# Kernel tuning notes

Hardware: AMD Instinct MI355X
Metric: run time of the kernel (lower is better)

## Reference

```python
import jax, jax.numpy as jnp
import numpy as np

N_NODES = 100000


def _graph_conv_right(feat, src, dst, W, b, n_nodes):
    # DGL GraphConv(norm='right'): since in_feats > out_feats, apply weight first,
    # then sum-aggregate messages over edges, divide by in-degree (clamped >= 1),
    # add bias, then relu activation.
    h = feat @ W                                   # [N, out]
    msg = jnp.take(h, src, axis=0)                 # [E, out] gather from source nodes
    agg = jax.ops.segment_sum(msg, dst, num_segments=n_nodes)  # [N, out]
    deg = jax.ops.segment_sum(jnp.ones_like(dst, dtype=feat.dtype), dst,
                              num_segments=n_nodes)
    deg = jnp.clip(deg, 1.0, None)                 # allow_zero_in_degree
    out = agg / deg[:, None] + b
    return jax.nn.relu(out)


def setup_inputs() -> dict:
    key = jax.random.key(0)
    ks = jax.random.split(key, 6)
    n_edges = 3200000
    in_dim, hidden_dim, out_dim = 128, 32, 12
    features = jax.random.normal(ks[0], (N_NODES, in_dim), dtype=jnp.float32)
    src = jax.random.randint(ks[1], (n_edges,), 0, N_NODES, dtype=jnp.int64 if jax.config.jax_enable_x64 else jnp.int32)
    dst = jax.random.randint(ks[2], (n_edges,), 0, N_NODES, dtype=jnp.int64 if jax.config.jax_enable_x64 else jnp.int32)
    W1 = jax.random.normal(ks[3], (in_dim, hidden_dim), dtype=jnp.float32) * (1.0 / np.sqrt(in_dim))
    b1 = jnp.zeros((hidden_dim,), dtype=jnp.float32)
    W2 = jax.random.normal(ks[4], (hidden_dim, out_dim), dtype=jnp.float32) * (1.0 / np.sqrt(hidden_dim))
    b2 = jnp.zeros((out_dim,), dtype=jnp.float32)
    return {"features": features, "src": src, "dst": dst,
            "W1": W1, "b1": b1, "W2": W2, "b2": b2}


def reference(features, src, dst, W1, b1, W2, b2):
    x = _graph_conv_right(features, src, dst, W1, b1, N_NODES)
    x = jax.nn.relu(x)  # extra F.relu after layer1 (idempotent, kept for fidelity)
    x = _graph_conv_right(x, src, dst, W2, b2, N_NODES)
    return x
```

## Files before the change

kernel.cpp:

```cpp
#include <hip/hip_runtime.h>
#include <hip/hip_fp16.h>

#define N_IN   128
#define HID    32
#define ODIM   12
#define RNODES 128
#define NBMAX  800
#define BCAP   4608
#define CHUNK  8192

__global__ __launch_bounds__(256) void gemm1_kernel(const float* __restrict__ feat,
                                                    const float* __restrict__ W1,
                                                    __half* __restrict__ h1, int nNodes) {
    __shared__ float sF[64 * 132];
    __shared__ float sW[N_IN * HID];
    const int tid = threadIdx.x;
    const int nb  = blockIdx.x * 64;

    {
        const float4* Wv  = (const float4*)W1;
        float4*       sWv = (float4*)sW;
        #pragma unroll
        for (int i = 0; i < 4; ++i) sWv[tid + 256 * i] = Wv[tid + 256 * i];
    }
    #pragma unroll
    for (int i = 0; i < 8; ++i) {
        int f   = tid + 256 * i;
        int row = f >> 5;
        int c4  = f & 31;
        int n   = nb + row;
        float4 v = make_float4(0.f, 0.f, 0.f, 0.f);
        if (n < nNodes) v = *(const float4*)(feat + (size_t)n * N_IN + c4 * 4);
        *(float4*)(sF + row * 132 + c4 * 4) = v;
    }
    __syncthreads();

    const int og = tid & 7;
    const int ng = tid >> 3;
    const int o0 = og * 4;
    const float* f0 = sF + ng * 132;
    const float* f1 = sF + (ng + 32) * 132;

    float acc0[4] = {0.f, 0.f, 0.f, 0.f};
    float acc1[4] = {0.f, 0.f, 0.f, 0.f};
    #pragma unroll 8
    for (int k = 0; k < N_IN; k += 4) {
        float4 a0 = *(const float4*)(f0 + k);
        float4 a1 = *(const float4*)(f1 + k);
        const float a0v[4] = {a0.x, a0.y, a0.z, a0.w};
        const float a1v[4] = {a1.x, a1.y, a1.z, a1.w};
        #pragma unroll
        for (int j = 0; j < 4; ++j) {
            float4 w = *(const float4*)(sW + (k + j) * HID + o0);
            acc0[0] += a0v[j] * w.x; acc0[1] += a0v[j] * w.y;
            acc0[2] += a0v[j] * w.z; acc0[3] += a0v[j] * w.w;
            acc1[0] += a1v[j] * w.x; acc1[1] += a1v[j] * w.y;
            acc1[2] += a1v[j] * w.z; acc1[3] += a1v[j] * w.w;
        }
    }
    int n0 = nb + ng, n1 = nb + ng + 32;
    if (n0 < nNodes) {
        union { __half2 h[2]; float2 f; } u;
        u.h[0] = __floats2half2_rn(acc0[0], acc0[1]);
        u.h[1] = __floats2half2_rn(acc0[2], acc0[3]);
        *(float2*)(h1 + (size_t)n0 * HID + o0) = u.f;
    }
    if (n1 < nNodes) {
        union { __half2 h[2]; float2 f; } u;
        u.h[0] = __floats2half2_rn(acc1[0], acc1[1]);
        u.h[1] = __floats2half2_rn(acc1[2], acc1[3]);
        *(float2*)(h1 + (size_t)n1 * HID + o0) = u.f;
    }
}

__global__ __launch_bounds__(256) void bplace_kernel(const int* __restrict__ src,
                                                     const int* __restrict__ dst,
                                                     int* __restrict__ bcur,
                                                     int* __restrict__ pairs, int nEdges) {
    __shared__ int lh[NBMAX];
    const int tid  = threadIdx.x;
    const int base = blockIdx.x * CHUNK;

    for (int b = tid; b < NBMAX; b += 256) lh[b] = 0;
    __syncthreads();

    #pragma unroll
    for (int j = 0; j < CHUNK / 1024; ++j) {
        int e = base + j * 1024 + tid * 4;
        if (e < nEdges) {
            int4 d = *(const int4*)(dst + e);
            atomicAdd(&lh[d.x >> 7], 1);
            atomicAdd(&lh[d.y >> 7], 1);
            atomicAdd(&lh[d.z >> 7], 1);
            atomicAdd(&lh[d.w >> 7], 1);
        }
    }
    __syncthreads();

    for (int b = tid; b < NBMAX; b += 256) {
        int c = lh[b];
        lh[b] = (c > 0) ? atomicAdd(&bcur[b], c) : 0;
    }
    __syncthreads();

    #pragma unroll
    for (int j = 0; j < CHUNK / 1024; ++j) {
        int e = base + j * 1024 + tid * 4;
        if (e < nEdges) {
            int4 d = *(const int4*)(dst + e);
            int4 s = *(const int4*)(src + e);
            int b0 = d.x >> 7, b1 = d.y >> 7, b2 = d.z >> 7, b3 = d.w >> 7;
            int p0 = atomicAdd(&lh[b0], 1);
            int p1 = atomicAdd(&lh[b1], 1);
            int p2 = atomicAdd(&lh[b2], 1);
            int p3 = atomicAdd(&lh[b3], 1);
            if (p0 < BCAP) pairs[(size_t)b0 * BCAP + p0] = ((d.x & 127) << 17) | s.x;
            if (p1 < BCAP) pairs[(size_t)b1 * BCAP + p1] = ((d.y & 127) << 17) | s.y;
            if (p2 < BCAP) pairs[(size_t)b2 * BCAP + p2] = ((d.z & 127) << 17) | s.z;
            if (p3 < BCAP) pairs[(size_t)b3 * BCAP + p3] = ((d.w & 127) << 17) | s.w;
        }
    }
}

__global__ __launch_bounds__(256) void bsort_kernel(const int* __restrict__ bcur,
                                                    int* __restrict__ pairs,
                                                    int* __restrict__ rowstart,
                                                    int* __restrict__ countg, int nNodes) {
    __shared__ int lp[BCAP];
    __shared__ int hist[RNODES];
    __shared__ int scn[RNODES];
    __shared__ int cur[RNODES];
    const int tid = threadIdx.x;
    const int bkt = blockIdx.x;
    const int cnt = min(bcur[bkt], BCAP);
    const size_t pb = (size_t)bkt * BCAP;

    if (tid < RNODES) hist[tid] = 0;
    __syncthreads();

    for (int i = tid; i < cnt; i += 256) {
        int v = pairs[pb + i];
        lp[i] = v;
        atomicAdd(&hist[v >> 17], 1);
    }
    __syncthreads();

    int v0 = (tid < RNODES) ? hist[tid] : 0;
    if (tid < RNODES) scn[tid] = v0;
    __syncthreads();
    int inc = v0;
    for (int off = 1; off < RNODES; off <<= 1) {
        int t = (tid < RNODES && tid >= off) ? scn[tid - off] : 0;
        __syncthreads();
        if (tid < RNODES) { inc += t; scn[tid] = inc; }
        __syncthreads();
    }
    if (tid < RNODES) {
        int excl = inc - v0;
        cur[tid] = excl;
        int n = bkt * RNODES + tid;
        if (n < nNodes) {
            rowstart[n] = (int)(pb + excl);
            countg[n]   = v0;
        }
    }
    __syncthreads();

    for (int i = tid; i < cnt; i += 256) {
        int v = lp[i];
        int pos = atomicAdd(&cur[v >> 17], 1);
        pairs[pb + pos] = v & 0x1FFFF;
    }
}

__global__ __launch_bounds__(256) void agg1_kernel(const __half* __restrict__ h1,
                                                   const int* __restrict__ rowstart,
                                                   const int* __restrict__ countg,
                                                   const int* __restrict__ eidx,
                                                   const float* __restrict__ b1,
                                                   const float* __restrict__ W2,
                                                   __half* __restrict__ h2,
                                                   float* __restrict__ rdeg, int nNodes) {
    __shared__ float sW2[HID * ODIM];
    const int tid = threadIdx.x;
    if (tid < 96) ((float4*)sW2)[tid] = ((const float4*)W2)[tid];
    __syncthreads();

    const int n = blockIdx.x * 16 + (tid >> 4);
    const int c = tid & 15;
    if (n >= nNodes) return;

    const int cnt = countg[n];
    const int beg = rowstart[n];
    const int end = beg + cnt;
    const __half2* h1v = (const __half2*)h1;

    float2 s0 = {0.f, 0.f}, s1 = {0.f, 0.f}, s2 = {0.f, 0.f}, s3 = {0.f, 0.f};
    int i = beg;
    for (; i + 4 <= end; i += 4) {
        int e0 = eidx[i], e1 = eidx[i + 1], e2 = eidx[i + 2], e3 = eidx[i + 3];
        float2 f0 = __half22float2(h1v[(size_t)e0 * 16 + c]);
        float2 f1 = __half22float2(h1v[(size_t)e1 * 16 + c]);
        float2 f2 = __half22float2(h1v[(size_t)e2 * 16 + c]);
        float2 f3 = __half22float2(h1v[(size_t)e3 * 16 + c]);
        s0.x += f0.x; s0.y += f0.y;
        s1.x += f1.x; s1.y += f1.y;
        s2.x += f2.x; s2.y += f2.y;
        s3.x += f3.x; s3.y += f3.y;
    }
    for (; i < end; ++i) {
        float2 f = __half22float2(h1v[(size_t)eidx[i] * 16 + c]);
        s0.x += f.x; s0.y += f.y;
    }
    float sumx = (s0.x + s1.x) + (s2.x + s3.x);
    float sumy = (s0.y + s1.y) + (s2.y + s3.y);

    float rd = 1.f / (float)(cnt < 1 ? 1 : cnt);
    float x0 = sumx * rd + b1[2 * c];
    float x1 = sumy * rd + b1[2 * c + 1];
    x0 = x0 > 0.f ? x0 : 0.f;
    x1 = x1 > 0.f ? x1 : 0.f;

    const int col = (c < ODIM) ? c : 0;
    float acc = 0.f;
    #pragma unroll
    for (int k = 0; k < 16; ++k) {
        float xk0 = __shfl(x0, k, 16);
        float xk1 = __shfl(x1, k, 16);
        acc += xk0 * sW2[(2 * k) * ODIM + col] + xk1 * sW2[(2 * k + 1) * ODIM + col];
    }
    if (c < ODIM) h2[(size_t)n * ODIM + c] = __float2half(acc);
    if (c == 0)   rdeg[n] = rd;
}

__global__ __launch_bounds__(256) void agg2_kernel(const __half* __restrict__ h2,
                                                   const int* __restrict__ rowstart,
                                                   const int* __restrict__ countg,
                                                   const int* __restrict__ eidx,
                                                   const float* __restrict__ rdeg,
                                                   const float* __restrict__ b2,
                                                   float* __restrict__ out, int nNodes) {
    const int tid = threadIdx.x;
    const int n = blockIdx.x * 32 + (tid >> 3);
    const int c = tid & 7;
    if (n >= nNodes) return;

    const int cnt = countg[n];
    const int beg = rowstart[n];
    const int end = beg + cnt;
    const int cc = (c < 6) ? c : 0;
    const __half2* h2v = (const __half2*)h2;

    float2 s0 = {0.f, 0.f}, s1 = {0.f, 0.f}, s2 = {0.f, 0.f}, s3 = {0.f, 0.f};
    int i = beg;
    for (; i + 4 <= end; i += 4) {
        int e0 = eidx[i], e1 = eidx[i + 1], e2 = eidx[i + 2], e3 = eidx[i + 3];
        float2 f0 = __half22float2(h2v[(size_t)e0 * 6 + cc]);
        float2 f1 = __half22float2(h2v[(size_t)e1 * 6 + cc]);
        float2 f2 = __half22float2(h2v[(size_t)e2 * 6 + cc]);
        float2 f3 = __half22float2(h2v[(size_t)e3 * 6 + cc]);
        s0.x += f0.x; s0.y += f0.y;
        s1.x += f1.x; s1.y += f1.y;
        s2.x += f2.x; s2.y += f2.y;
        s3.x += f3.x; s3.y += f3.y;
    }
    for (; i < end; ++i) {
        float2 f = __half22float2(h2v[(size_t)eidx[i] * 6 + cc]);
        s0.x += f.x; s0.y += f.y;
    }
    float sumx = (s0.x + s1.x) + (s2.x + s3.x);
    float sumy = (s0.y + s1.y) + (s2.y + s3.y);

    float rd = rdeg[n];
    float v0 = sumx * rd + b2[2 * cc];
    float v1 = sumy * rd + b2[2 * cc + 1];
    v0 = v0 > 0.f ? v0 : 0.f;
    v1 = v1 > 0.f ? v1 : 0.f;
    if (c < 6) *(float2*)(out + (size_t)n * ODIM + 2 * c) = make_float2(v0, v1);
}

extern "C" void kernel_launch(void* const* d_in, const int* in_sizes, int n_in,
                              void* d_out, int out_size, void* d_ws, size_t ws_size,
                              hipStream_t stream) {
    const float* feat = (const float*)d_in[0];
    const int*   src  = (const int*)d_in[1];
    const int*   dst  = (const int*)d_in[2];
    const float* W1   = (const float*)d_in[3];
    const float* b1   = (const float*)d_in[4];
    const float* W2   = (const float*)d_in[5];
    const float* b2   = (const float*)d_in[6];
    float* out = (float*)d_out;

    const int nEdges = in_sizes[1];
    const int nNodes = in_sizes[0] / N_IN;
    const int nb     = (nNodes + RNODES - 1) / RNODES;

    __half* h1      = (__half*)d_ws;
    __half* h2      = h1 + (size_t)nNodes * HID;
    float* rdeg     = (float*)(h2 + (size_t)nNodes * ODIM);
    int*   rowstart = (int*)(rdeg + nNodes);
    int*   countg   = rowstart + nNodes;
    int*   bcur     = countg + nNodes;
    int*   pairs    = bcur + NBMAX;

    hipMemsetAsync(bcur, 0, NBMAX * sizeof(int), stream);

    gemm1_kernel<<<(nNodes + 63) / 64, 256, 0, stream>>>(feat, W1, h1, nNodes);
    bplace_kernel<<<(nEdges + CHUNK - 1) / CHUNK, 256, 0, stream>>>(src, dst, bcur, pairs, nEdges);
    bsort_kernel<<<nb, 256, 0, stream>>>(bcur, pairs, rowstart, countg, nNodes);
    agg1_kernel<<<(nNodes + 15) / 16, 256, 0, stream>>>(h1, rowstart, countg, pairs, b1, W2, h2, rdeg, nNodes);
    agg2_kernel<<<(nNodes + 31) / 32, 256, 0, stream>>>(h2, rowstart, countg, pairs, rdeg, b2, out, nNodes);
}
```

Baseline: 272.9 us.

## Fuse bucket sort into aggregation kernels and stage bucket placement in LDS

Drops the separate bsort kernel. Each aggregation kernel now loads its bucket of (dst,src) pairs, counting-sorts them in shared memory and aggregates one 128-node bucket per block. bplace now does a block-local scan and stages entries in LDS grouped by bucket before scattering, so global writes are more contiguous. In exchange the counting sort is done twice (once in each agg kernel), and with only about 782 large blocks per agg kernel there is less parallelism across the GPU.

After: 238.9 us. -12.4%, faster.

```diff
diff --git a/kernel.cpp b/kernel.cpp
--- a/kernel.cpp
+++ b/kernel.cpp
@@ -6,8 +6,9 @@
 #define ODIM   12
 #define RNODES 128
 #define NBMAX  800
+#define NBK2   1024
 #define BCAP   4608
-#define CHUNK  8192
+#define CHUNK  4096
 
 __global__ __launch_bounds__(256) void gemm1_kernel(const float* __restrict__ feat,
                                                     const float* __restrict__ W1,
@@ -73,60 +74,191 @@
     }
 }
 
-__global__ __launch_bounds__(256) void bplace_kernel(const int* __restrict__ src,
+__global__ __launch_bounds__(512) void bplace_kernel(const int* __restrict__ src,
                                                      const int* __restrict__ dst,
                                                      int* __restrict__ bcur,
                                                      int* __restrict__ pairs, int nEdges) {
-    __shared__ int lh[NBMAX];
+    __shared__ int      lh[NBK2];
+    __shared__ int      lcur[NBK2];
+    __shared__ int      gofs[NBK2];
+    __shared__ int      sAux[512];
+    __shared__ int      lst[CHUNK];
+    __shared__ unsigned short lbk[CHUNK];
+
     const int tid  = threadIdx.x;
     const int base = blockIdx.x * CHUNK;
-
-    for (int b = tid; b < NBMAX; b += 256) lh[b] = 0;
-    __syncthreads();
-
-    #pragma unroll
-    for (int j = 0; j < CHUNK / 1024; ++j) {
-        int e = base + j * 1024 + tid * 4;
-        if (e < nEdges) {
-            int4 d = *(const int4*)(dst + e);
-            atomicAdd(&lh[d.x >> 7], 1);
-            atomicAdd(&lh[d.y >> 7], 1);
-            atomicAdd(&lh[d.z >> 7], 1);
-            atomicAdd(&lh[d.w >> 7], 1);
-        }
-    }
-    __syncthreads();
-
-    for (int b = tid; b < NBMAX; b += 256) {
-        int c = lh[b];
-        lh[b] = (c > 0) ? atomicAdd(&bcur[b], c) : 0;
-    }
-    __syncthreads();
-
-    #pragma unroll
-    for (int j = 0; j < CHUNK / 1024; ++j) {
-        int e = base + j * 1024 + tid * 4;
-        if (e < nEdges) {
-            int4 d = *(const int4*)(dst + e);
-            int4 s = *(const int4*)(src + e);
-            int b0 = d.x >> 7, b1 = d.y >> 7, b2 = d.z >> 7, b3 = d.w >> 7;
-            int p0 = atomicAdd(&lh[b0], 1);
-            int p1 = atomicAdd(&lh[b1], 1);
-            int p2 = atomicAdd(&lh[b2], 1);
-            int p3 = atomicAdd(&lh[b3], 1);
-            if (p0 < BCAP) pairs[(size_t)b0 * BCAP + p0] = ((d.x & 127) << 17) | s.x;
-            if (p1 < BCAP) pairs[(size_t)b1 * BCAP + p1] = ((d.y & 127) << 17) | s.y;
-            if (p2 < BCAP) pairs[(size_t)b2 * BCAP + p2] = ((d.z & 127) << 17) | s.z;
-            if (p3 < BCAP) pairs[(size_t)b3 * BCAP + p3] = ((d.w & 127) << 17) | s.w;
-        }
-    }
-}
-
-__global__ __launch_bounds__(256) void bsort_kernel(const int* __restrict__ bcur,
-                                                    int* __restrict__ pairs,
-                                                    int* __restrict__ rowstart,
-                                                    int* __restrict__ countg, int nNodes) {
-    __shared__ int lp[BCAP];
+    const int m    = min(CHUNK, nEdges - base);
+
+    lh[tid] = 0; lh[tid + 512] = 0;
+    __syncthreads();
+
+    int4 dv[2], sv[2];
+    bool ok[2];
+    #pragma unroll
+    for (int k = 0; k < 2; ++k) {
+        int e = base + k * 2048 + tid * 4;
+        ok[k] = (e < nEdges);
+        if (ok[k]) {
+            dv[k] = *(const int4*)(dst + e);
+            sv[k] = *(const int4*)(src + e);
+        }
+    }
+    #pragma unroll
+    for (int k = 0; k < 2; ++k) {
+        if (ok[k]) {
+            atomicAdd(&lh[dv[k].x >> 7], 1);
+            atomicAdd(&lh[dv[k].y >> 7], 1);
+            atomicAdd(&lh[dv[k].z >> 7], 1);
+            atomicAdd(&lh[dv[k].w >> 7], 1);
+        }
+    }
+    __syncthreads();
+
+    int c0 = lh[2 * tid], c1 = lh[2 * tid + 1];
+    int tsum = c0 + c1;
+    sAux[tid] = tsum;
+    __syncthreads();
+    int inc = tsum;
+    for (int off = 1; off < 512; off <<= 1) {
+        int t = (tid >= off) ? sAux[tid - off] : 0;
+        __syncthreads();
+        inc += t;
+        sAux[tid] = inc;
+        __syncthreads();
+    }
+    int excl = inc - tsum;
+    lh[2 * tid]     = excl;
+    lh[2 * tid + 1] = excl + c0;
+    lcur[2 * tid]     = excl;
+    lcur[2 * tid + 1] = excl + c0;
+    gofs[2 * tid]     = (c0 > 0) ? atomicAdd(&bcur[2 * tid], c0) : 0;
+    gofs[2 * tid + 1] = (c1 > 0) ? atomicAdd(&bcur[2 * tid + 1], c1) : 0;
+    __syncthreads();
+
+    #pragma unroll
+    for (int k = 0; k < 2; ++k) {
+        if (ok[k]) {
+            int b, p;
+            b = dv[k].x >> 7; p = atomicAdd(&lcur[b], 1); lst[p] = ((dv[k].x & 127) << 17) | sv[k].x; lbk[p] = (unsigned short)b;
+            b = dv[k].y >> 7; p = atomicAdd(&lcur[b], 1); lst[p] = ((dv[k].y & 127) << 17) | sv[k].y; lbk[p] = (unsigned short)b;
+            b = dv[k].z >> 7; p = atomicAdd(&lcur[b], 1); lst[p] = ((dv[k].z & 127) << 17) | sv[k].z; lbk[p] = (unsigned short)b;
+            b = dv[k].w >> 7; p = atomicAdd(&lcur[b], 1); lst[p] = ((dv[k].w & 127) << 17) | sv[k].w; lbk[p] = (unsigned short)b;
+        }
+    }
+    __syncthreads();
+
+    for (int i = tid; i < m; i += 512) {
+        int b = lbk[i];
+        int cap = gofs[b] + (i - lh[b]);
+        if (cap < (b + 1) * BCAP - (b * BCAP) + 0) {}
+        int rank = gofs[b] + (i - lh[b]);
+        if (rank < BCAP) pairs[(size_t)b * BCAP + rank] = lst[i];
+    }
+}
+
+__global__ __launch_bounds__(512) void agg1_kernel(const __half* __restrict__ h1,
+                                                   const int* __restrict__ bcur,
+                                                   const int* __restrict__ pairs,
+                                                   const float* __restrict__ b1,
+                                                   const float* __restrict__ W2,
+                                                   __half* __restrict__ h2,
+                                                   float* __restrict__ rdeg, int nNodes) {
+    __shared__ int   sorted[BCAP];
+    __shared__ int   hist[RNODES];
+    __shared__ int   scn[RNODES];
+    __shared__ int   cur[RNODES];
+    __shared__ float sW2[HID * ODIM];
+    const int tid = threadIdx.x;
+    const int bkt = blockIdx.x;
+    const int cnt = min(bcur[bkt], BCAP);
+    const size_t pb = (size_t)bkt * BCAP;
+
+    if (tid < RNODES) hist[tid] = 0;
+    if (tid < 96) ((float4*)sW2)[tid] = ((const float4*)W2)[tid];
+    __syncthreads();
+
+    for (int i = tid; i < cnt; i += 512) atomicAdd(&hist[pairs[pb + i] >> 17], 1);
+    __syncthreads();
+
+    int v0 = (tid < RNODES) ? hist[tid] : 0;
+    if (tid < RNODES) scn[tid] = v0;
+    __syncthreads();
+    int inc = v0;
+    for (int off = 1; off < RNODES; off <<= 1) {
+        int t = (tid < RNODES && tid >= off) ? scn[tid - off] : 0;
+        __syncthreads();
+        if (tid < RNODES) { inc += t; scn[tid] = inc; }
+        __syncthreads();
+    }
+    if (tid < RNODES) { scn[tid] = inc - v0; cur[tid] = inc - v0; }
+    __syncthreads();
+
+    for (int i = tid; i < cnt; i += 512) {
+        int v = pairs[pb + i];
+        int pos = atomicAdd(&cur[v >> 17], 1);
+        sorted[pos] = v & 0x1FFFF;
+    }
+    __syncthreads();
+
+    const int c   = tid & 15;
+    const int grp = tid >> 4;
+    const __half2* h1v = (const __half2*)h1;
+    const int col = (c < ODIM) ? c : 0;
+
+    #pragma unroll
+    for (int g = 0; g < 4; ++g) {
+        int nl = g * 32 + grp;
+        int n  = bkt * RNODES + nl;
+        if (n >= nNodes) continue;
+        int dcnt = hist[nl];
+        int beg  = scn[nl];
+        int end  = beg + dcnt;
+
+        float2 s0 = {0.f, 0.f}, s1 = {0.f, 0.f}, s2 = {0.f, 0.f}, s3 = {0.f, 0.f};
+        int i = beg;
+        for (; i + 4 <= end; i += 4) {
+            int e0 = sorted[i], e1 = sorted[i + 1], e2 = sorted[i + 2], e3 = sorted[i + 3];
+            float2 f0 = __half22float2(h1v[(size_t)e0 * 16 + c]);
+            float2 f1 = __half22float2(h1v[(size_t)e1 * 16 + c]);
+            float2 f2 = __half22float2(h1v[(size_t)e2 * 16 + c]);
+            float2 f3 = __half22float2(h1v[(size_t)e3 * 16 + c]);
+            s0.x += f0.x; s0.y += f0.y;
+            s1.x += f1.x; s1.y += f1.y;
+            s2.x += f2.x; s2.y += f2.y;
+            s3.x += f3.x; s3.y += f3.y;
+        }
+        for (; i < end; ++i) {
+            float2 f = __half22float2(h1v[(size_t)sorted[i] * 16 + c]);
+            s0.x += f.x; s0.y += f.y;
+        }
+        float sumx = (s0.x + s1.x) + (s2.x + s3.x);
+        float sumy = (s0.y + s1.y) + (s2.y + s3.y);
+
+        float rd = 1.f / (float)(dcnt < 1 ? 1 : dcnt);
+        float x0 = sumx * rd + b1[2 * c];
+        float x1 = sumy * rd + b1[2 * c + 1];
+        x0 = x0 > 0.f ? x0 : 0.f;
+        x1 = x1 > 0.f ? x1 : 0.f;
+
+        float acc = 0.f;
+        #pragma unroll
+        for (int k = 0; k < 16; ++k) {
+            float xk0 = __shfl(x0, k, 16);
+            float xk1 = __shfl(x1, k, 16);
+            acc += xk0 * sW2[(2 * k) * ODIM + col] + xk1 * sW2[(2 * k + 1) * ODIM + col];
+        }
+        if (c < ODIM) h2[(size_t)n * ODIM + c] = __float2half(acc);
+        if (c == 0)   rdeg[n] = rd;
+    }
+}
+
+__global__ __launch_bounds__(512) void agg2_kernel(const __half* __restrict__ h2,
+                                                   const int* __restrict__ bcur,
+                                                   const int* __restrict__ pairs,
+                                                   const float* __restrict__ rdeg,
+                                                   const float* __restrict__ b2,
+                                                   float* __restrict__ out, int nNodes) {
+    __shared__ int sorted[BCAP];
     __shared__ int hist[RNODES];
     __shared__ int scn[RNODES];
     __shared__ int cur[RNODES];
@@ -138,11 +270,7 @@
     if (tid < RNODES) hist[tid] = 0;
     __syncthreads();
 
-    for (int i = tid; i < cnt; i += 256) {
-        int v = pairs[pb + i];
-        lp[i] = v;
-        atomicAdd(&hist[v >> 17], 1);
-    }
+    for (int i = tid; i < cnt; i += 512) atomicAdd(&hist[pairs[pb + i] >> 17], 1);
     __syncthreads();
 
     int v0 = (tid < RNODES) ? hist[tid] : 0;
@@ -155,128 +283,57 @@
         if (tid < RNODES) { inc += t; scn[tid] = inc; }
         __syncthreads();
     }
-    if (tid < RNODES) {
-        int excl = inc - v0;
-        cur[tid] = excl;
-        int n = bkt * RNODES + tid;
-        if (n < nNodes) {
-            rowstart[n] = (int)(pb + excl);
-            countg[n]   = v0;
-        }
-    }
-    __syncthreads();
-
-    for (int i = tid; i < cnt; i += 256) {
-        int v = lp[i];
+    if (tid < RNODES) { scn[tid] = inc - v0; cur[tid] = inc - v0; }
+    __syncthreads();
+
+    for (int i = tid; i < cnt; i += 512) {
+        int v = pairs[pb + i];
         int pos = atomicAdd(&cur[v >> 17], 1);
-        pairs[pb + pos] = v & 0x1FFFF;
-    }
-}
-
-__global__ __launch_bounds__(256) void agg1_kernel(const __half* __restrict__ h1,
-                                                   const int* __restrict__ rowstart,
-                                                   const int* __restrict__ countg,
-                                                   const int* __restrict__ eidx,
-                                                   const float* __restrict__ b1,
-                                                   const float* __restrict__ W2,
-                                                   __half* __restrict__ h2,
-                                                   float* __restrict__ rdeg, int nNodes) {
-    __shared__ float sW2[HID * ODIM];
-    const int tid = threadIdx.x;
-    if (tid < 96) ((float4*)sW2)[tid] = ((const float4*)W2)[tid];
-    __syncthreads();
-
-    const int n = blockIdx.x * 16 + (tid >> 4);
-    const int c = tid & 15;
-    if (n >= nNodes) return;
-
-    const int cnt = countg[n];
-    const int beg = rowstart[n];
-    const int end = beg + cnt;
-    const __half2* h1v = (const __half2*)h1;
-
-    float2 s0 = {0.f, 0.f}, s1 = {0.f, 0.f}, s2 = {0.f, 0.f}, s3 = {0.f, 0.f};
-    int i = beg;
-    for (; i + 4 <= end; i += 4) {
-        int e0 = eidx[i], e1 = eidx[i + 1], e2 = eidx[i + 2], e3 = eidx[i + 3];
-        float2 f0 = __half22float2(h1v[(size_t)e0 * 16 + c]);
-        float2 f1 = __half22float2(h1v[(size_t)e1 * 16 + c]);
-        float2 f2 = __half22float2(h1v[(size_t)e2 * 16 + c]);
-        float2 f3 = __half22float2(h1v[(size_t)e3 * 16 + c]);
-        s0.x += f0.x; s0.y += f0.y;
-        s1.x += f1.x; s1.y += f1.y;
-        s2.x += f2.x; s2.y += f2.y;
-        s3.x += f3.x; s3.y += f3.y;
-    }
-    for (; i < end; ++i) {
-        float2 f = __half22float2(h1v[(size_t)eidx[i] * 16 + c]);
-        s0.x += f.x; s0.y += f.y;
-    }
-    float sumx = (s0.x + s1.x) + (s2.x + s3.x);
-    float sumy = (s0.y + s1.y) + (s2.y + s3.y);
-
-    float rd = 1.f / (float)(cnt < 1 ? 1 : cnt);
-    float x0 = sumx * rd + b1[2 * c];
-    float x1 = sumy * rd + b1[2 * c + 1];
-    x0 = x0 > 0.f ? x0 : 0.f;
-    x1 = x1 > 0.f ? x1 : 0.f;
-
-    const int col = (c < ODIM) ? c : 0;
-    float acc = 0.f;
-    #pragma unroll
-    for (int k = 0; k < 16; ++k) {
-        float xk0 = __shfl(x0, k, 16);
-        float xk1 = __shfl(x1, k, 16);
-        acc += xk0 * sW2[(2 * k) * ODIM + col] + xk1 * sW2[(2 * k + 1) * ODIM + col];
-    }
-    if (c < ODIM) h2[(size_t)n * ODIM + c] = __float2half(acc);
-    if (c == 0)   rdeg[n] = rd;
-}
-
-__global__ __launch_bounds__(256) void agg2_kernel(const __half* __restrict__ h2,
-                                                   const int* __restrict__ rowstart,
-                                                   const int* __restrict__ countg,
-                                                   const int* __restrict__ eidx,
-                                                   const float* __restrict__ rdeg,
-                                                   const float* __restrict__ b2,
-                                                   float* __restrict__ out, int nNodes) {
-    const int tid = threadIdx.x;
-    const int n = blockIdx.x * 32 + (tid >> 3);
-    const int c = tid & 7;
-    if (n >= nNodes) return;
-
-    const int cnt = countg[n];
-    const int beg = rowstart[n];
-    const int end = beg + cnt;
-    const int cc = (c < 6) ? c : 0;
+        sorted[pos] = v & 0x1FFFF;
+    }
+    __syncthreads();
+
+    const int c   = tid & 7;
+    const int grp = tid >> 3;
+    const int cc  = (c < 6) ? c : 0;
     const __half2* h2v = (const __half2*)h2;
 
-    float2 s0 = {0.f, 0.f}, s1 = {0.f, 0.f}, s2 = {0.f, 0.f}, s3 = {0.f, 0.f};
-    int i = beg;
-    for (; i + 4 <= end; i += 4) {
-        int e0 = eidx[i], e1 = eidx[i + 1], e2 = eidx[i + 2], e3 = eidx[i + 3];
-        float2 f0 = __half22float2(h2v[(size_t)e0 * 6 + cc]);
-        float2 f1 = __half22float2(h2v[(size_t)e1 * 6 + cc]);
-        float2 f2 = __half22float2(h2v[(size_t)e2 * 6 + cc]);
-        float2 f3 = __half22float2(h2v[(size_t)e3 * 6 + cc]);
-        s0.x += f0.x; s0.y += f0.y;
-        s1.x += f1.x; s1.y += f1.y;
-        s2.x += f2.x; s2.y += f2.y;
-        s3.x += f3.x; s3.y += f3.y;
-    }
-    for (; i < end; ++i) {
-        float2 f = __half22float2(h2v[(size_t)eidx[i] * 6 + cc]);
-        s0.x += f.x; s0.y += f.y;
-    }
-    float sumx = (s0.x + s1.x) + (s2.x + s3.x);
-    float sumy = (s0.y + s1.y) + (s2.y + s3.y);
-
-    float rd = rdeg[n];
-    float v0 = sumx * rd + b2[2 * cc];
-    float v1 = sumy * rd + b2[2 * cc + 1];
-    v0 = v0 > 0.f ? v0 : 0.f;
-    v1 = v1 > 0.f ? v1 : 0.f;
-    if (c < 6) *(float2*)(out + (size_t)n * ODIM + 2 * c) = make_float2(v0, v1);
+    #pragma unroll
+    for (int g = 0; g < 2; ++g) {
+        int nl = g * 64 + grp;
+        int n  = bkt * RNODES + nl;
+        if (n >= nNodes) continue;
+        int dcnt = hist[nl];
+        int beg  = scn[nl];
+        int end  = beg + dcnt;
+
+        float2 s0 = {0.f, 0.f}, s1 = {0.f, 0.f}, s2 = {0.f, 0.f}, s3 = {0.f, 0.f};
+        int i = beg;
+        for (; i + 4 <= end; i += 4) {
+            int e0 = sorted[i], e1 = sorted[i + 1], e2 = sorted[i + 2], e3 = sorted[i + 3];
+            float2 f0 = __half22float2(h2v[(size_t)e0 * 6 + cc]);
+            float2 f1 = __half22float2(h2v[(size_t)e1 * 6 + cc]);
+            float2 f2 = __half22float2(h2v[(size_t)e2 * 6 + cc]);
+            float2 f3 = __half22float2(h2v[(size_t)e3 * 6 + cc]);
+            s0.x += f0.x; s0.y += f0.y;
+            s1.x += f1.x; s1.y += f1.y;
+            s2.x += f2.x; s2.y += f2.y;
+            s3.x += f3.x; s3.y += f3.y;
+        }
+        for (; i < end; ++i) {
+            float2 f = __half22float2(h2v[(size_t)sorted[i] * 6 + cc]);
+            s0.x += f.x; s0.y += f.y;
+        }
+        float sumx = (s0.x + s1.x) + (s2.x + s3.x);
+        float sumy = (s0.y + s1.y) + (s2.y + s3.y);
+
+        float rd = rdeg[n];
+        float w0 = sumx * rd + b2[2 * cc];
+        float w1 = sumy * rd + b2[2 * cc + 1];
+        w0 = w0 > 0.f ? w0 : 0.f;
+        w1 = w1 > 0.f ? w1 : 0.f;
+        if (c < 6) *(float2*)(out + (size_t)n * ODIM + 2 * c) = make_float2(w0, w1);
+    }
 }
 
 extern "C" void kernel_launch(void* const* d_in, const int* in_sizes, int n_in,
@@ -295,19 +352,16 @@
     const int nNodes = in_sizes[0] / N_IN;
     const int nb     = (nNodes + RNODES - 1) / RNODES;
 
-    __half* h1      = (__half*)d_ws;
-    __half* h2      = h1 + (size_t)nNodes * HID;
-    float* rdeg     = (float*)(h2 + (size_t)nNodes * ODIM);
-    int*   rowstart = (int*)(rdeg + nNodes);
-    int*   countg   = rowstart + nNodes;
-    int*   bcur     = countg + nNodes;
-    int*   pairs    = bcur + NBMAX;
-
-    hipMemsetAsync(bcur, 0, NBMAX * sizeof(int), stream);
+    __half* h1   = (__half*)d_ws;
+    __half* h2   = h1 + (size_t)nNodes * HID;
+    float*  rdeg = (float*)(h2 + (size_t)nNodes * ODIM);
+    int*    bcur = (int*)(rdeg + nNodes);
+    int*    pairs = bcur + NBK2;
+
+    hipMemsetAsync(bcur, 0, NBK2 * sizeof(int), stream);
 
     gemm1_kernel<<<(nNodes + 63) / 64, 256, 0, stream>>>(feat, W1, h1, nNodes);
-    bplace_kernel<<<(nEdges + CHUNK - 1) / CHUNK, 256, 0, stream>>>(src, dst, bcur, pairs, nEdges);
-    bsort_kernel<<<nb, 256, 0, stream>>>(bcur, pairs, rowstart, countg, nNodes);
-    agg1_kernel<<<(nNodes + 15) / 16, 256, 0, stream>>>(h1, rowstart, countg, pairs, b1, W2, h2, rdeg, nNodes);
-    agg2_kernel<<<(nNodes + 31) / 32, 256, 0, stream>>>(h2, rowstart, countg, pairs, rdeg, b2, out, nNodes);
-}
+    bplace_kernel<<<(nEdges + CHUNK - 1) / CHUNK, 512, 0, stream>>>(src, dst, bcur, pairs, nEdges);
+    agg1_kernel<<<nb, 512, 0, stream>>>(h1, bcur, pairs, b1, W2, h2, rdeg, nNodes);
+    agg2_kernel<<<nb, 512, 0, stream>>>(h2, bcur, pairs, rdeg, b2, out, nNodes);
+}
```
